# Kernel tuning notes

Measured on AMD Instinct MI355X. Metric: run time of the kernel, lower is better.

Reference implementation:

```python
import jax, jax.numpy as jnp
import numpy as np

D = 1024

def setup_inputs() -> dict:
    key = jax.random.key(0)
    ks = jax.random.split(key, 7)
    s = 1.0 / np.sqrt(D)
    return {
        "x": jax.random.normal(ks[0], (4, 2048, D), dtype=jnp.float32),
        "Wq": jax.random.uniform(ks[1], (D, D), jnp.float32, -s, s),
        "bq": jax.random.uniform(ks[2], (D,), jnp.float32, -s, s),
        "Wk": jax.random.uniform(ks[3], (D, D), jnp.float32, -s, s),
        "bk": jax.random.uniform(ks[4], (D,), jnp.float32, -s, s),
        "Wv": jax.random.uniform(ks[5], (D, D), jnp.float32, -s, s),
        "bv": jax.random.uniform(ks[6], (D,), jnp.float32, -s, s),
    }

def reference(x, Wq, bq, Wk, bk, Wv, bv):
    # x: [B, S, D]
    q = jnp.einsum('bsd,de->bse', x, Wq.T) + bq
    k = jnp.einsum('bsd,de->bse', x, Wk.T) + bk
    v = jnp.einsum('bsd,de->bse', x, Wv.T) + bv
    scale = 1.0 / jnp.sqrt(jnp.float32(x.shape[-1]))
    score = jnp.einsum('bqd,bkd->bqk', q, k) * scale  # [B, S, S]
    attn = jax.nn.softmax(score, axis=-1)
    return jnp.einsum('bqk,bkd->bqd', attn, v)
```

## Files before the change

### kernel.cpp

```cpp
#include <hip/hip_runtime.h>

typedef short shortx8 __attribute__((ext_vector_type(8)));
typedef float floatx4 __attribute__((ext_vector_type(4)));
typedef unsigned short ushortx4 __attribute__((ext_vector_type(4)));
typedef unsigned short ushortx8 __attribute__((ext_vector_type(8)));

typedef __attribute__((address_space(1))) char gchar;
typedef __attribute__((address_space(3))) char lchar;

__device__ __forceinline__ void async16(const void* g, void* l) {
    __builtin_amdgcn_global_load_lds((gchar*)g, (lchar*)l, 16, 0, 0);
}

__device__ __forceinline__ unsigned short f2bf(float f) {
    union { float f; unsigned int u; } v;
    v.f = f;
    unsigned int r = v.u + 0x7fffu + ((v.u >> 16) & 1u);
    return (unsigned short)(r >> 16);
}

__device__ __forceinline__ float bf2f(unsigned short h) {
    union { unsigned int u; float f; } v;
    v.u = ((unsigned int)h) << 16;
    return v.f;
}

__device__ __forceinline__ void gemm_mainloop(const ushort* __restrict__ Arow,
                                              const ushort* __restrict__ Brow,
                                              int K, ushort* As, ushort* Bs,
                                              floatx4 acc[4][4]) {
    const int t = threadIdx.x;
    const int w = t >> 6;
    const int lane = t & 63;
    const size_t ldb = (size_t)K * 2;
    const int frs = lane >> 3;
    const int kql = (lane & 7) ^ (lane >> 4);
    const char* gA0 = (const char*)Arow + (size_t)(32 * w + frs) * ldb + (kql << 4);
    const char* gA1 = (const char*)Arow + (size_t)(32 * w + 8 + frs) * ldb + ((kql ^ 4) << 4);
    const char* gB0 = (const char*)Brow + (size_t)(32 * w + frs) * ldb + (kql << 4);
    const char* gB1 = (const char*)Brow + (size_t)(32 * w + 8 + frs) * ldb + ((kql ^ 4) << 4);
    char* lA = (char*)As + w * 4096;
    char* lB = (char*)Bs + w * 4096;
    const int ga0 = (w & 1) * 4;
    const int gb0 = (w >> 1) * 4;
    const int fr = lane & 15;
    const int kq = lane >> 4;
    const int xr = (fr >> 1) & 7;
    const int loff0 = fr * 128 + ((kq ^ xr) << 4);
    const int loff1 = fr * 128 + (((kq + 4) ^ xr) << 4);
    const int nk = K >> 6;
    for (int kt = 0; kt < nk; ++kt) {
        async16(gA0,            lA);
        async16(gA1,            lA + 1024);
        async16(gA0 + 16 * ldb, lA + 2048);
        async16(gA1 + 16 * ldb, lA + 3072);
        async16(gB0,            lB);
        async16(gB1,            lB + 1024);
        async16(gB0 + 16 * ldb, lB + 2048);
        async16(gB1 + 16 * ldb, lB + 3072);
        gA0 += 128; gA1 += 128; gB0 += 128; gB1 += 128;
        __syncthreads();
        shortx8 a0[4], b0[4], a1[4], b1[4];
#pragma unroll
        for (int i = 0; i < 4; ++i) {
            a0[i] = *(const shortx8*)((const char*)As + (ga0 + i) * 2048 + loff0);
            a1[i] = *(const shortx8*)((const char*)As + (ga0 + i) * 2048 + loff1);
        }
#pragma unroll
        for (int j = 0; j < 4; ++j) {
            b0[j] = *(const shortx8*)((const char*)Bs + (gb0 + j) * 2048 + loff0);
            b1[j] = *(const shortx8*)((const char*)Bs + (gb0 + j) * 2048 + loff1);
        }
#pragma unroll
        for (int i = 0; i < 4; ++i)
#pragma unroll
            for (int j = 0; j < 4; ++j)
                acc[i][j] = __builtin_amdgcn_mfma_f32_16x16x32_bf16(a0[i], b0[j], acc[i][j], 0, 0, 0);
#pragma unroll
        for (int i = 0; i < 4; ++i)
#pragma unroll
            for (int j = 0; j < 4; ++j)
                acc[i][j] = __builtin_amdgcn_mfma_f32_16x16x32_bf16(a1[i], b1[j], acc[i][j], 0, 0, 0);
        __syncthreads();
    }
}

template<int JN>
__device__ __forceinline__ void gemm256_mainloop(
        const ushort* __restrict__ Arow, const ushort* __restrict__ Brow,
        int K, ushort* ldsp, floatx4 (&acc)[8][JN])
{
    const int t = threadIdx.x;
    const int w = t >> 6;
    const int lane = t & 63;
    const size_t ldb = (size_t)K * 2;
    constexpr int ABYTES = 32768;
    constexpr int BBYTES = JN * 8192;
    constexpr int BUFB = ABYTES + BBYTES;
    char* l0 = (char*)ldsp;
    const int wst = w << 10;
    const int sc = (((t & 7) ^ ((t >> 4) & 7)) << 4);
    const char* gA = (const char*)Arow + (size_t)(t >> 3) * ldb + sc;
    const char* gB = (const char*)Brow + (size_t)(t >> 3) * ldb + sc;
    const int fr = lane & 15, kq = lane >> 4;
    const int xr = (fr >> 1) & 7;
    const int ck0 = (kq ^ xr) << 4;
    const int ck1 = ((kq + 4) ^ xr) << 4;
    const int wm = w & 1, wn = w >> 1;
    const int abase = (wm * 128 + fr) * 128;
    const int bbase = (wn * (JN * 16) + fr) * 128;

#define STA(buf, kt, R) async16(gA + (size_t)(R) * ldb + (size_t)(kt) * 128, \
                                l0 + (buf) * BUFB + (R) * 128 + wst)
#define STB(buf, kt, R) async16(gB + (size_t)(R) * ldb + (size_t)(kt) * 128, \
                                l0 + (buf) * BUFB + ABYTES + (R) * 128 + wst)
#define LDA4(buf, mb, ck)                                                          \
    a0 = *(const shortx8*)(l0 + (buf) * BUFB + abase + ((mb) + 0) * 2048 + (ck));  \
    a1 = *(const shortx8*)(l0 + (buf) * BUFB + abase + ((mb) + 1) * 2048 + (ck));  \
    a2 = *(const shortx8*)(l0 + (buf) * BUFB + abase + ((mb) + 2) * 2048 + (ck));  \
    a3 = *(const shortx8*)(l0 + (buf) * BUFB + abase + ((mb) + 3) * 2048 + (ck));
#define LDB(buf, ck, dst)                                                          \
    _Pragma("unroll")                                                              \
    for (int n = 0; n < JN; ++n)                                                   \
        dst[n] = *(const shortx8*)(l0 + (buf) * BUFB + ABYTES + bbase + n * 2048 + (ck));
#define PH(MB, BV)                                                                 \
    __builtin_amdgcn_s_setprio(1);                                                 \
    _Pragma("unroll")                                                              \
    for (int n = 0; n < JN; ++n) {                                                 \
        acc[(MB) + 0][n] = __builtin_amdgcn_mfma_f32_16x16x32_bf16(a0, BV[n], acc[(MB) + 0][n], 0, 0, 0); \
        acc[(MB) + 1][n] = __builtin_amdgcn_mfma_f32_16x16x32_bf16(a1, BV[n], acc[(MB) + 1][n], 0, 0, 0); \
        acc[(MB) + 2][n] = __builtin_amdgcn_mfma_f32_16x16x32_bf16(a2, BV[n], acc[(MB) + 2][n], 0, 0, 0); \
        acc[(MB) + 3][n] = __builtin_amdgcn_mfma_f32_16x16x32_bf16(a3, BV[n], acc[(MB) + 3][n], 0, 0, 0); \
    }                                                                              \
    __builtin_amdgcn_s_setprio(0);
#define PH_OPEN()                                                      \
    __builtin_amdgcn_sched_barrier(0);                                 \
    __builtin_amdgcn_s_barrier();                                      \
    asm volatile("s_waitcnt lgkmcnt(0)" ::: "memory");                 \
    __builtin_amdgcn_sched_barrier(0);
#define PH_CLOSE() __builtin_amdgcn_s_barrier();
#define VMW_A()                                                        \
    asm volatile("s_waitcnt vmcnt(%0)" :: "i"(JN + 4) : "memory");     \
    __builtin_amdgcn_s_barrier();                                      \
    __builtin_amdgcn_sched_barrier(0);
#define VMW_B()                                                        \
    asm volatile("s_waitcnt vmcnt(%0)" :: "i"(JN + 2) : "memory");     \
    __builtin_amdgcn_s_barrier();                                      \
    __builtin_amdgcn_sched_barrier(0);

    const int nk = K >> 6;
    const int nit = nk >> 1;

    STA(0, 0, 0); STA(0, 0, 128);
    STB(0, 0, 0); STB(0, 0, 64);
    if (JN == 4) { STB(0, 0, 128); STB(0, 0, 192); }
    STA(0, 0, 64); STA(0, 0, 192);
    STB(1, 1, 0); STB(1, 1, 64);
    if (JN == 4) { STB(1, 1, 128); STB(1, 1, 192); }
    asm volatile("s_waitcnt vmcnt(%0)" :: "i"(JN + 2) : "memory");
    __builtin_amdgcn_s_barrier();
    __builtin_amdgcn_sched_barrier(0);

    shortx8 a0, a1, a2, a3;
    shortx8 b0[JN], b1[JN];

    for (int it = 0; it < nit; ++it) {
        const int T = 2 * it;
        const int T1 = T + 1;
        int T2 = T + 2; if (T2 > nk - 1) T2 = nk - 1;
        int T3 = T + 3; if (T3 > nk - 1) T3 = nk - 1;

        LDA4(0, 0, ck0); LDB(0, ck0, b0);
        STA(1, T1, 0); STA(1, T1, 128);
        PH_OPEN();
        PH(0, b0);
        PH_CLOSE();

        LDA4(0, 0, ck1); LDB(0, ck1, b1);
        STA(1, T1, 64); STA(1, T1, 192);
        PH_OPEN();
        PH(0, b1);
        VMW_A();

        LDA4(0, 4, ck0);
        STB(0, T2, 0); STB(0, T2, 64);
        PH_OPEN();
        PH(4, b0);
        PH_CLOSE();

        LDA4(0, 4, ck1);
        if (JN == 4) { STB(0, T2, 128); STB(0, T2, 192); }
        PH_OPEN();
        PH(4, b1);
        VMW_B();

        LDA4(1, 0, ck0); LDB(1, ck0, b0);
        STA(0, T2, 0); STA(0, T2, 128);
        PH_OPEN();
        PH(0, b0);
        PH_CLOSE();

        LDA4(1, 0, ck1); LDB(1, ck1, b1);
        STA(0, T2, 64); STA(0, T2, 192);
        PH_OPEN();
        PH(0, b1);
        VMW_A();

        LDA4(1, 4, ck0);
        STB(1, T3, 0); STB(1, T3, 64);
        PH_OPEN();
        PH(4, b0);
        PH_CLOSE();

        LDA4(1, 4, ck1);
        if (JN == 4) { STB(1, T3, 128); STB(1, T3, 192); }
        PH_OPEN();
        PH(4, b1);
        VMW_B();
    }
#undef STA
#undef STB
#undef LDA4
#undef LDB
#undef PH
#undef PH_OPEN
#undef PH_CLOSE
#undef VMW_A
#undef VMW_B
}

__global__ __launch_bounds__(256, 3)
void qkv_gemm(const ushort* __restrict__ xb, const ushort* __restrict__ Wb,
              const float* __restrict__ bq, const float* __restrict__ bk,
              const float* __restrict__ bv,
              ushort* __restrict__ Qs, ushort* __restrict__ Ks,
              ushort* __restrict__ Vt) {
    __shared__ __align__(16) ushort lds[16384];
    const int mbase = blockIdx.y * 128;
    const int nglob = blockIdx.x * 128;
    const int z = nglob >> 10;
    const int nbase = nglob & 1023;
    floatx4 acc[4][4];
    const floatx4 zero = {0.0f, 0.0f, 0.0f, 0.0f};
#pragma unroll
    for (int i = 0; i < 4; ++i)
#pragma unroll
        for (int j = 0; j < 4; ++j) acc[i][j] = zero;

    gemm_mainloop(xb + (size_t)mbase * 1024, Wb + (size_t)nglob * 1024,
                  1024, lds, lds + 8192, acc);

    const int t = threadIdx.x, w = t >> 6, lane = t & 63;
    const int mw = (w & 1) * 64, nw = (w >> 1) * 64;
    const int r0 = mbase + mw + (lane >> 4) * 4;
    const int c0 = nbase + nw + (lane & 15);
    const float* bias = (z == 0) ? bq : (z == 1) ? bk : bv;
    const float scale = (z == 0) ? 0.03125f : 1.0f;
    float bj[4];
#pragma unroll
    for (int j = 0; j < 4; ++j) bj[j] = bias[c0 + j * 16];

    if (z < 2) {
        ushort* O = (z == 0) ? Qs : Ks;
#pragma unroll
        for (int i = 0; i < 4; ++i)
#pragma unroll
            for (int j = 0; j < 4; ++j)
#pragma unroll
                for (int r = 0; r < 4; ++r) {
                    int gr = r0 + i * 16 + r;
                    int gc = c0 + j * 16;
                    O[(size_t)gr * 1024 + gc] = f2bf((acc[i][j][r] + bj[j]) * scale);
                }
    } else {
#pragma unroll
        for (int i = 0; i < 4; ++i)
#pragma unroll
            for (int j = 0; j < 4; ++j)
#pragma unroll
                for (int r = 0; r < 4; ++r) {
                    int gr = r0 + i * 16 + r;
                    int gc = c0 + j * 16;
                    Vt[(size_t)(gr >> 11) * (1024 * 2048) + (size_t)gc * 2048 + (gr & 2047)] =
                        f2bf(acc[i][j][r] + bj[j]);
                }
    }
}

__global__ __launch_bounds__(512, 2)
void s_gemm_exp(const ushort* __restrict__ A, size_t sAz,
                const ushort* __restrict__ B, size_t sBz,
                ushort* __restrict__ C, size_t sCz,
                float* __restrict__ rowsum, int N, int K) {
    __shared__ __align__(16) ushort lds[65536];
    const int mbase = blockIdx.y * 256;
    const int nbase = blockIdx.x * 256;
    const int z = blockIdx.z;
    floatx4 acc[8][4];
    const floatx4 zero = {0.0f, 0.0f, 0.0f, 0.0f};
#pragma unroll
    for (int i = 0; i < 8; ++i)
#pragma unroll
        for (int j = 0; j < 4; ++j) acc[i][j] = zero;

    gemm256_mainloop<4>(A + z * sAz + (size_t)mbase * K,
                        B + z * sBz + (size_t)nbase * K, K, lds, acc);

    const int t = threadIdx.x, w = t >> 6, lane = t & 63;
    const int wm = w & 1, wn = w >> 1;
    const int r0 = mbase + wm * 128 + (lane >> 4) * 4;
    const int c0 = nbase + wn * 64 + (lane & 15);
    ushort* Cz = C + z * sCz;
    float* rsz = rowsum + z * 2048;

#pragma unroll
    for (int i = 0; i < 8; ++i)
#pragma unroll
        for (int j = 0; j < 4; ++j)
#pragma unroll
            for (int r = 0; r < 4; ++r) {
                float e = __expf(acc[i][j][r]);
                acc[i][j][r] = e;
                Cz[(size_t)(r0 + i * 16 + r) * N + (c0 + j * 16)] = f2bf(e);
            }

#pragma unroll
    for (int i = 0; i < 8; ++i)
#pragma unroll
        for (int r = 0; r < 4; ++r) {
            float s = acc[i][0][r] + acc[i][1][r] + acc[i][2][r] + acc[i][3][r];
            s += __shfl_xor(s, 1);
            s += __shfl_xor(s, 2);
            s += __shfl_xor(s, 4);
            s += __shfl_xor(s, 8);
            if ((lane & 15) == 0) atomicAdd(rsz + (r0 + i * 16 + r), s);
        }
}

__global__ __launch_bounds__(512, 2)
void pv_gemm(const ushort* __restrict__ A, size_t sAz,
             const ushort* __restrict__ B, size_t sBz,
             float* __restrict__ C, size_t sCz,
             const float* __restrict__ rowsum, int N, int K) {
    __shared__ __align__(16) ushort lds[49152];
    const int mbase = blockIdx.y * 256;
    const int nbase = blockIdx.x * 128;
    const int z = blockIdx.z;
    floatx4 acc[8][2];
    const floatx4 zero = {0.0f, 0.0f, 0.0f, 0.0f};
#pragma unroll
    for (int i = 0; i < 8; ++i)
#pragma unroll
        for (int j = 0; j < 2; ++j) acc[i][j] = zero;

    gemm256_mainloop<2>(A + z * sAz + (size_t)mbase * K,
                        B + z * sBz + (size_t)nbase * K, K, lds, acc);

    const int t = threadIdx.x, w = t >> 6, lane = t & 63;
    const int wm = w & 1, wn = w >> 1;
    const int r0 = mbase + wm * 128 + (lane >> 4) * 4;
    const int c0 = nbase + wn * 32 + (lane & 15);
    float* Cz = C + z * sCz;
    const float* rsz = rowsum + z * 2048;
#pragma unroll
    for (int i = 0; i < 8; ++i)
#pragma unroll
        for (int r = 0; r < 4; ++r) {
            const float inv = 1.0f / rsz[r0 + i * 16 + r];
#pragma unroll
            for (int j = 0; j < 2; ++j)
                Cz[(size_t)(r0 + i * 16 + r) * N + (c0 + j * 16)] = acc[i][j][r] * inv;
        }
}

__global__ __launch_bounds__(256)
void cast_bf16_all(const float* __restrict__ x, const float* __restrict__ Wq,
                   const float* __restrict__ Wk, const float* __restrict__ Wv,
                   ushort* __restrict__ dst, float* __restrict__ rowsum) {
    const int NX = 2097152;
    const int NW = 262144;
    const int bi = blockIdx.x;
    if (bi >= 11264) {
        int k = (bi - 11264) * 256 + threadIdx.x;
        float4 zz = {0.0f, 0.0f, 0.0f, 0.0f};
        ((float4*)rowsum)[k] = zz;
        return;
    }
    int i = bi * 256 + threadIdx.x;
    const float* src;
    int off;
    if (i < NX)               { src = x;  off = 0; }
    else if (i < NX + NW)     { src = Wq; off = NX; }
    else if (i < NX + 2 * NW) { src = Wk; off = NX + NW; }
    else                      { src = Wv; off = NX + 2 * NW; }
    float4 v = ((const float4*)src)[i - off];
    ushortx4 o = {f2bf(v.x), f2bf(v.y), f2bf(v.z), f2bf(v.w)};
    ((ushortx4*)dst)[i] = o;
}

extern "C" void kernel_launch(void* const* d_in, const int* in_sizes, int n_in,
                              void* d_out, int out_size, void* d_ws, size_t ws_size,
                              hipStream_t stream) {
    const float* x  = (const float*)d_in[0];
    const float* bq = (const float*)d_in[2];
    const float* bk = (const float*)d_in[4];
    const float* bv = (const float*)d_in[6];
    float* out = (float*)d_out;

    const size_t R = 8192;
    const size_t D = 1024;
    const size_t S = 2048;

    const size_t need = (4 * R * D + 3 * D * D + 4 * S * S) * 2 + 4 * S * 4;
    if (ws_size < need) return;

    ushort* xb = (ushort*)d_ws;
    ushort* Wb = xb + R * D;
    ushort* Qs = Wb + 3 * D * D;
    ushort* Ks = Qs + R * D;
    ushort* Vt = Ks + R * D;
    ushort* Sb = Vt + R * D;
    float* rowsum = (float*)(Sb + 4 * S * S);

    cast_bf16_all<<<dim3(11272), dim3(256), 0, stream>>>(
        x, (const float*)d_in[1], (const float*)d_in[3], (const float*)d_in[5], xb, rowsum);

    qkv_gemm<<<dim3(24, 64), dim3(256), 0, stream>>>(xb, Wb, bq, bk, bv, Qs, Ks, Vt);

    s_gemm_exp<<<dim3(8, 8, 4), dim3(512), 0, stream>>>(Qs, S * D, Ks, S * D, Sb, S * S,
                                                        rowsum, (int)S, (int)D);

    pv_gemm<<<dim3(8, 8, 4), dim3(512), 0, stream>>>(Sb, S * S, Vt, D * S, out, S * D,
                                                     rowsum, (int)D, (int)S);
}
```

Baseline: 244.6 us.

## Fuse all attention stages into one persistent cooperative kernel with grid syncs

Replaces the four kernel launches (cast, QKV GEMM, S=exp(QK^T) GEMM, PV GEMM) with a single cooperative persistent kernel of 768 blocks that runs each stage in turn, separated by grid-wide syncs. The goal is to remove launch overhead and the gaps between kernels. In exchange, every stage now uses the smaller 128x128 gemm_mainloop tile with 256 threads instead of the tuned 256-wide kernels. The PV stage also uses only 512 of the 768 blocks, and grid syncs add their own cost. The old four-kernel path remains as a fallback if the cooperative launch fails.

Result: slower. 518.1 us (+111.8%).

```diff
diff --git a/kernel.cpp b/kernel.cpp
--- a/kernel.cpp
+++ b/kernel.cpp
@@ -1,4 +1,7 @@
 #include <hip/hip_runtime.h>
+#include <hip/hip_cooperative_groups.h>
+
+namespace cg = cooperative_groups;
 
 typedef short shortx8 __attribute__((ext_vector_type(8)));
 typedef float floatx4 __attribute__((ext_vector_type(4)));
@@ -82,6 +85,184 @@
             for (int j = 0; j < 4; ++j)
                 acc[i][j] = __builtin_amdgcn_mfma_f32_16x16x32_bf16(a1[i], b1[j], acc[i][j], 0, 0, 0);
         __syncthreads();
+    }
+}
+
+__global__ __launch_bounds__(256, 3)
+void attn_fused(const float* __restrict__ x,
+                const float* __restrict__ Wqf, const float* __restrict__ Wkf,
+                const float* __restrict__ Wvf,
+                const float* __restrict__ bq, const float* __restrict__ bk,
+                const float* __restrict__ bv,
+                ushort* __restrict__ xb,
+                ushort* __restrict__ Qs, ushort* __restrict__ Ks,
+                ushort* __restrict__ Vt, ushort* __restrict__ Sb,
+                float* __restrict__ rowsum, float* __restrict__ out)
+{
+    __shared__ __align__(16) ushort lds[16384];
+    const int bid = blockIdx.x;
+    const int tid = threadIdx.x;
+
+    {
+        const int NX = 2097152;
+        const int NW = 262144;
+        const int NT = NX + 3 * NW;
+        const int NZ = 512;
+        for (int i = bid * 256 + tid; i < NT + NZ; i += 768 * 256) {
+            if (i < NT) {
+                const float* src; int off;
+                if (i < NX)               { src = x;   off = 0; }
+                else if (i < NX + NW)     { src = Wqf; off = NX; }
+                else if (i < NX + 2 * NW) { src = Wkf; off = NX + NW; }
+                else                      { src = Wvf; off = NX + 2 * NW; }
+                float4 v = ((const float4*)src)[i - off];
+                ushortx4 o = {f2bf(v.x), f2bf(v.y), f2bf(v.z), f2bf(v.w)};
+                ((ushortx4*)xb)[i] = o;
+            } else {
+                float4 zz = {0.0f, 0.0f, 0.0f, 0.0f};
+                ((float4*)rowsum)[i - NT] = zz;
+            }
+        }
+    }
+    cg::this_grid().sync();
+
+    {
+        const ushort* Wb = xb + (size_t)8192 * 1024;
+        for (int rr = 0; rr < 2; ++rr) {
+            const int vb = bid + rr * 768;
+            const int bx = vb % 24, by = vb / 24;
+            const int mbase = by * 128;
+            const int nglob = bx * 128;
+            const int z = nglob >> 10;
+            const int nbase = nglob & 1023;
+            floatx4 acc[4][4];
+            const floatx4 zero = {0.0f, 0.0f, 0.0f, 0.0f};
+#pragma unroll
+            for (int i = 0; i < 4; ++i)
+#pragma unroll
+                for (int j = 0; j < 4; ++j) acc[i][j] = zero;
+
+            gemm_mainloop(xb + (size_t)mbase * 1024, Wb + (size_t)nglob * 1024,
+                          1024, lds, lds + 8192, acc);
+
+            const int w = tid >> 6, lane = tid & 63;
+            const int mw = (w & 1) * 64, nw = (w >> 1) * 64;
+            const int r0 = mbase + mw + (lane >> 4) * 4;
+            const int c0 = nbase + nw + (lane & 15);
+            const float* bias = (z == 0) ? bq : (z == 1) ? bk : bv;
+            const float scale = (z == 0) ? 0.03125f : 1.0f;
+            float bj[4];
+#pragma unroll
+            for (int j = 0; j < 4; ++j) bj[j] = bias[c0 + j * 16];
+
+            if (z < 2) {
+                ushort* O = (z == 0) ? Qs : Ks;
+#pragma unroll
+                for (int i = 0; i < 4; ++i)
+#pragma unroll
+                    for (int j = 0; j < 4; ++j)
+#pragma unroll
+                        for (int r = 0; r < 4; ++r) {
+                            int gr = r0 + i * 16 + r;
+                            int gc = c0 + j * 16;
+                            O[(size_t)gr * 1024 + gc] = f2bf((acc[i][j][r] + bj[j]) * scale);
+                        }
+            } else {
+#pragma unroll
+                for (int i = 0; i < 4; ++i)
+#pragma unroll
+                    for (int j = 0; j < 4; ++j)
+#pragma unroll
+                        for (int r = 0; r < 4; ++r) {
+                            int gr = r0 + i * 16 + r;
+                            int gc = c0 + j * 16;
+                            Vt[(size_t)(gr >> 11) * (1024 * 2048) + (size_t)gc * 2048 + (gr & 2047)] =
+                                f2bf(acc[i][j][r] + bj[j]);
+                        }
+            }
+        }
+    }
+    cg::this_grid().sync();
+
+    {
+        for (int vb = bid; vb < 1024; vb += 768) {
+            const int z = vb >> 8;
+            const int rem = vb & 255;
+            const int bx = rem & 15, by = rem >> 4;
+            const ushort* Az = Qs + (size_t)z * 2048 * 1024 + (size_t)by * 128 * 1024;
+            const ushort* Bz = Ks + (size_t)z * 2048 * 1024 + (size_t)bx * 128 * 1024;
+            floatx4 acc[4][4];
+            const floatx4 zero = {0.0f, 0.0f, 0.0f, 0.0f};
+#pragma unroll
+            for (int i = 0; i < 4; ++i)
+#pragma unroll
+                for (int j = 0; j < 4; ++j) acc[i][j] = zero;
+
+            gemm_mainloop(Az, Bz, 1024, lds, lds + 8192, acc);
+
+            const int w = tid >> 6, lane = tid & 63;
+            const int mw = (w & 1) * 64, nw = (w >> 1) * 64;
+            const int r0 = by * 128 + mw + (lane >> 4) * 4;
+            const int c0 = bx * 128 + nw + (lane & 15);
+            ushort* Cz = Sb + (size_t)z * 2048 * 2048;
+            float* rsz = rowsum + z * 2048;
+
+#pragma unroll
+            for (int i = 0; i < 4; ++i)
+#pragma unroll
+                for (int j = 0; j < 4; ++j)
+#pragma unroll
+                    for (int r = 0; r < 4; ++r) {
+                        float e = __expf(acc[i][j][r]);
+                        acc[i][j][r] = e;
+                        Cz[(size_t)(r0 + i * 16 + r) * 2048 + (c0 + j * 16)] = f2bf(e);
+                    }
+#pragma unroll
+            for (int i = 0; i < 4; ++i)
+#pragma unroll
+                for (int r = 0; r < 4; ++r) {
+                    float s = acc[i][0][r] + acc[i][1][r] + acc[i][2][r] + acc[i][3][r];
+                    s += __shfl_xor(s, 1);
+                    s += __shfl_xor(s, 2);
+                    s += __shfl_xor(s, 4);
+                    s += __shfl_xor(s, 8);
+                    if ((lane & 15) == 0) atomicAdd(rsz + (r0 + i * 16 + r), s);
+                }
+        }
+    }
+    cg::this_grid().sync();
+
+    if (bid < 512) {
+        const int vb = bid;
+        const int z = vb >> 7;
+        const int rem = vb & 127;
+        const int bx = rem & 7, by = rem >> 3;
+        const ushort* Az = Sb + (size_t)z * 2048 * 2048 + (size_t)by * 128 * 2048;
+        const ushort* Bz = Vt + (size_t)z * 1024 * 2048 + (size_t)bx * 128 * 2048;
+        floatx4 acc[4][4];
+        const floatx4 zero = {0.0f, 0.0f, 0.0f, 0.0f};
+#pragma unroll
+        for (int i = 0; i < 4; ++i)
+#pragma unroll
+            for (int j = 0; j < 4; ++j) acc[i][j] = zero;
+
+        gemm_mainloop(Az, Bz, 2048, lds, lds + 8192, acc);
+
+        const int w = tid >> 6, lane = tid & 63;
+        const int mw = (w & 1) * 64, nw = (w >> 1) * 64;
+        const int r0 = by * 128 + mw + (lane >> 4) * 4;
+        const int c0 = bx * 128 + nw + (lane & 15);
+        float* Cz = out + (size_t)z * 2048 * 1024;
+        const float* rsz = rowsum + z * 2048;
+#pragma unroll
+        for (int i = 0; i < 4; ++i)
+#pragma unroll
+            for (int r = 0; r < 4; ++r) {
+                const float inv = 1.0f / rsz[r0 + i * 16 + r];
+#pragma unroll
+                for (int j = 0; j < 4; ++j)
+                    Cz[(size_t)(r0 + i * 16 + r) * 1024 + (c0 + j * 16)] = acc[i][j][r] * inv;
+            }
     }
 }
 
@@ -172,51 +353,35 @@
 
         LDA4(0, 0, ck0); LDB(0, ck0, b0);
         STA(1, T1, 0); STA(1, T1, 128);
-        PH_OPEN();
-        PH(0, b0);
-        PH_CLOSE();
+        PH_OPEN(); PH(0, b0); PH_CLOSE();
 
         LDA4(0, 0, ck1); LDB(0, ck1, b1);
         STA(1, T1, 64); STA(1, T1, 192);
-        PH_OPEN();
-        PH(0, b1);
-        VMW_A();
+        PH_OPEN(); PH(0, b1); VMW_A();
 
         LDA4(0, 4, ck0);
         STB(0, T2, 0); STB(0, T2, 64);
-        PH_OPEN();
-        PH(4, b0);
-        PH_CLOSE();
+        PH_OPEN(); PH(4, b0); PH_CLOSE();
 
         LDA4(0, 4, ck1);
         if (JN == 4) { STB(0, T2, 128); STB(0, T2, 192); }
-        PH_OPEN();
-        PH(4, b1);
-        VMW_B();
+        PH_OPEN(); PH(4, b1); VMW_B();
 
         LDA4(1, 0, ck0); LDB(1, ck0, b0);
         STA(0, T2, 0); STA(0, T2, 128);
-        PH_OPEN();
-        PH(0, b0);
-        PH_CLOSE();
+        PH_OPEN(); PH(0, b0); PH_CLOSE();
 
         LDA4(1, 0, ck1); LDB(1, ck1, b1);
         STA(0, T2, 64); STA(0, T2, 192);
-        PH_OPEN();
-        PH(0, b1);
-        VMW_A();
+        PH_OPEN(); PH(0, b1); VMW_A();
 
         LDA4(1, 4, ck0);
         STB(1, T3, 0); STB(1, T3, 64);
-        PH_OPEN();
-        PH(4, b0);
-        PH_CLOSE();
+        PH_OPEN(); PH(4, b0); PH_CLOSE();
 
         LDA4(1, 4, ck1);
         if (JN == 4) { STB(1, T3, 128); STB(1, T3, 192); }
-        PH_OPEN();
-        PH(4, b1);
-        VMW_B();
+        PH_OPEN(); PH(4, b1); VMW_B();
     }
 #undef STA
 #undef STB
@@ -323,7 +488,6 @@
                 acc[i][j][r] = e;
                 Cz[(size_t)(r0 + i * 16 + r) * N + (c0 + j * 16)] = f2bf(e);
             }
-
 #pragma unroll
     for (int i = 0; i < 8; ++i)
 #pragma unroll
@@ -401,10 +565,13 @@
 extern "C" void kernel_launch(void* const* d_in, const int* in_sizes, int n_in,
                               void* d_out, int out_size, void* d_ws, size_t ws_size,
                               hipStream_t stream) {
-    const float* x  = (const float*)d_in[0];
-    const float* bq = (const float*)d_in[2];
-    const float* bk = (const float*)d_in[4];
-    const float* bv = (const float*)d_in[6];
+    const float* x   = (const float*)d_in[0];
+    const float* Wqf = (const float*)d_in[1];
+    const float* bq  = (const float*)d_in[2];
+    const float* Wkf = (const float*)d_in[3];
+    const float* bk  = (const float*)d_in[4];
+    const float* Wvf = (const float*)d_in[5];
+    const float* bv  = (const float*)d_in[6];
     float* out = (float*)d_out;
 
     const size_t R = 8192;
@@ -422,14 +589,19 @@
     ushort* Sb = Vt + R * D;
     float* rowsum = (float*)(Sb + 4 * S * S);
 
-    cast_bf16_all<<<dim3(11272), dim3(256), 0, stream>>>(
-        x, (const float*)d_in[1], (const float*)d_in[3], (const float*)d_in[5], xb, rowsum);
-
+    void* args[] = {(void*)&x, (void*)&Wqf, (void*)&Wkf, (void*)&Wvf,
+                    (void*)&bq, (void*)&bk, (void*)&bv,
+                    (void*)&xb, (void*)&Qs, (void*)&Ks, (void*)&Vt, (void*)&Sb,
+                    (void*)&rowsum, (void*)&out};
+    hipError_t err = hipLaunchCooperativeKernel((const void*)attn_fused,
+                                                dim3(768), dim3(256),
+                                                args, 0, stream);
+    if (err == hipSuccess) return;
+
+    cast_bf16_all<<<dim3(11272), dim3(256), 0, stream>>>(x, Wqf, Wkf, Wvf, xb, rowsum);
     qkv_gemm<<<dim3(24, 64), dim3(256), 0, stream>>>(xb, Wb, bq, bk, bv, Qs, Ks, Vt);
-
     s_gemm_exp<<<dim3(8, 8, 4), dim3(512), 0, stream>>>(Qs, S * D, Ks, S * D, Sb, S * S,
                                                         rowsum, (int)S, (int)D);
-
     pv_gemm<<<dim3(8, 8, 4), dim3(512), 0, stream>>>(Sb, S * S, Vt, D * S, out, S * D,
                                                      rowsum, (int)D, (int)S);
 }
```
